# Optimization experiments

Hardware: AMD Instinct MI355X
Metric: run time of the kernel (lower is better)

The kernel has to match this reference:

```python
import jax, jax.numpy as jnp
import numpy as np

GH, GW = 8, 8  # hypernetwork patch grid
EPS = 1e-5


def image_coords(b, h, w, dtype):
    # matches get_image_coordinates: channel0 = x (varies along W), channel1 = y (varies along H)
    xs = jnp.linspace(-1.0, 1.0, w, dtype=dtype)
    ys = jnp.linspace(-1.0, 1.0, h, dtype=dtype)
    X = jnp.broadcast_to(xs[None, :], (h, w))
    Y = jnp.broadcast_to(ys[:, None], (h, w))
    g = jnp.stack([X, Y], axis=0)  # [2,H,W]
    return jnp.broadcast_to(g[None], (b, 2, h, w))


def im2col3(x):
    # reflect-pad 3x3 im2col -> [B,C,9,H,W]
    H, W = x.shape[2], x.shape[3]
    xp = jnp.pad(x, ((0, 0), (0, 0), (1, 1), (1, 1)), mode='reflect')
    cols = [xp[:, :, i:i + H, j:j + W] for i in range(3) for j in range(3)]
    return jnp.stack(cols, axis=2)


def meta_dw3(x, wsig):
    # depthwise 3x3 conv with per-patch weights. wsig: [B, C*9, GH, GW]
    B, C, H, W = x.shape
    p, q = H // GH, W // GW
    cols = im2col3(x).reshape(B, C, 9, GH, p, GW, q)
    Wd = wsig.reshape(B, C, 9, GH, GW)
    out = jnp.einsum('bctuivj,bctuv->bcuivj', cols, Wd)
    return out.reshape(B, C, H, W)


def meta_pw(x, wsig, out_nc):
    # pointwise 1x1 conv with per-patch weights. wsig: [B, out_nc*C, GH, GW]
    B, C, H, W = x.shape
    p, q = H // GH, W // GW
    xr = x.reshape(B, C, GH, p, GW, q)
    Wp = wsig.reshape(B, out_nc, C, GH, GW)
    out = jnp.einsum('bcuivj,bocuv->bouivj', xr, Wp)
    return out.reshape(B, out_nc, H, W)


def batch_norm(x, g, b):
    m = jnp.mean(x, (0, 2, 3), keepdims=True)
    v = jnp.var(x, (0, 2, 3), keepdims=True)
    return (x - m) * jax.lax.rsqrt(v + EPS) * g[None, :, None, None] + b[None, :, None, None]


def relu6(x):
    return jnp.clip(x, 0.0, 6.0)


def hpir(x, wsig, out_nc, g_dw, b_dw, g_pw, b_pw):
    # HyperPatchInvertedResidual, expand_ratio=1, stride=1, in_nc != out_nc -> no residual
    C = x.shape[1]
    n_dw = C * 9
    h = relu6(batch_norm(meta_dw3(x, wsig[:, :n_dw]), g_dw, b_dw))
    h = batch_norm(meta_pw(h, wsig[:, n_dw:n_dw + out_nc * C], out_nc), g_pw, b_pw)
    return h


def resize_bilinear(p, hw):
    B, C = p.shape[0], p.shape[1]
    return jax.image.resize(p, (B, C, hw[0], hw[1]), method='bilinear')


def decoder_forward(x_img, f0, f1, w0, w1, w2,
                    g_dw0, b_dw0, g_pw0, b_pw0,
                    g_dw1, b_dw1, g_pw1, b_pw1,
                    g_dw2, b_dw2, g_pw2, b_pw2):
    feats = [x_img, f0, f1]  # [img] + features[:-1]
    level_w = [w0, w1, w2]
    level_out = [64, 32, 21]
    bn_p = [(g_dw0, b_dw0, g_pw0, b_pw0),
            (g_dw1, b_dw1, g_pw1, b_pw1),
            (g_dw2, b_dw2, g_pw2, b_pw2)]
    p = None
    for level in range(3):
        f = feats[-level - 1]
        if p is None:
            p = f
        else:
            if p.shape[2:] != f.shape[2:]:
                p = resize_bilinear(p, f.shape[2:])
            p = jnp.concatenate([f, p], axis=1)
        B, _, H, W = p.shape
        p = jnp.concatenate([image_coords(B, H, W, p.dtype), p], axis=1)
        g_dw, b_dw, g_pw, b_pw = bn_p[level]
        p = hpir(p, level_w[level], level_out[level], g_dw, b_dw, g_pw, b_pw)
    return p


def setup_inputs() -> dict:
    key = jax.random.key(0)
    ks = jax.random.split(key, 8)
    inp = {
        'x_img': jax.random.normal(ks[0], (4, 3, 256, 256), jnp.float32),
        'f0': jax.random.normal(ks[1], (4, 32, 64, 64), jnp.float32),
        'f1': jax.random.normal(ks[2], (4, 64, 32, 32), jnp.float32),
        'w0': jax.random.normal(ks[3], (4, 4818, 8, 8), jnp.float32) * 0.1,
        'w1': jax.random.normal(ks[4], (4, 4018, 8, 8), jnp.float32) * 0.1,
        'w2': jax.random.normal(ks[5], (4, 1110, 8, 8), jnp.float32) * 0.1,
    }
    for name, c in [('dw0', 66), ('pw0', 64), ('dw1', 98), ('pw1', 32), ('dw2', 37), ('pw2', 21)]:
        inp['g_' + name] = jnp.ones((c,), jnp.float32)
        inp['b_' + name] = jnp.zeros((c,), jnp.float32)
    return inp


def reference(x_img, f0, f1, w0, w1, w2,
              g_dw0, b_dw0, g_pw0, b_pw0,
              g_dw1, b_dw1, g_pw1, b_pw1,
              g_dw2, b_dw2, g_pw2, b_pw2):
    return decoder_forward(x_img, f0, f1, w0, w1, w2,
                           g_dw0, b_dw0, g_pw0, b_pw0,
                           g_dw1, b_dw1, g_pw1, b_pw1,
                           g_dw2, b_dw2, g_pw2, b_pw2)
```

## Files before the change

kernel.cpp:

```cpp
#include <hip/hip_runtime.h>

#define EPS 1e-5f

__device__ __forceinline__ int reflect_idx(int i, int n) {
    if (i < 0) return -i;
    if (i >= n) return 2 * n - 2 - i;
    return i;
}

__device__ __forceinline__ float bilin(const float* __restrict__ pb, int Hp, float sy, float sx) {
    int y0 = (int)floorf(sy), x0 = (int)floorf(sx);
    float fy = sy - y0, fx = sx - x0;
    int y0c = min(max(y0, 0), Hp - 1), y1c = min(max(y0 + 1, 0), Hp - 1);
    int x0c = min(max(x0, 0), Hp - 1), x1c = min(max(x0 + 1, 0), Hp - 1);
    float v00 = pb[y0c * Hp + x0c], v01 = pb[y0c * Hp + x1c];
    float v10 = pb[y1c * Hp + x0c], v11 = pb[y1c * Hp + x1c];
    return v00 * (1 - fy) * (1 - fx) + v01 * (1 - fy) * fx
         + v10 * fy * (1 - fx) + v11 * fy * fx;
}

template <int C>
__device__ __forceinline__ void reduce_ss_wide(const float* __restrict__ part,
                                               const float* __restrict__ g,
                                               const float* __restrict__ bb,
                                               float* ss, float* scratch,
                                               float invN, int tid) {
    constexpr int G = 256 / C;
    int grp = tid / C;
    int c = tid - grp * C;
    if (grp < G) {
        float s1 = 0.f, s2 = 0.f;
        for (int s = grp; s < 64; s += G) {
            s1 += part[s * 2 * C + 2 * c];
            s2 += part[s * 2 * C + 2 * c + 1];
        }
        scratch[grp * 2 * C + 2 * c] = s1;
        scratch[grp * 2 * C + 2 * c + 1] = s2;
    }
    __syncthreads();
    if (tid < C) {
        float s1 = 0.f, s2 = 0.f;
#pragma unroll
        for (int gg = 0; gg < G; ++gg) {
            s1 += scratch[gg * 2 * C + 2 * tid];
            s2 += scratch[gg * 2 * C + 2 * tid + 1];
        }
        float m = s1 * invN;
        float var = s2 * invN - m * m;
        float sc = g[tid] * rsqrtf(var + EPS);
        ss[2 * tid] = sc;
        ss[2 * tid + 1] = bb[tid] - m * sc;
    }
    __syncthreads();
}

__global__ __launch_bounds__(256)
void wtrans_kernel(const float* __restrict__ w2, float* __restrict__ wT) {
    int uv = blockIdx.x & 63, b = blockIdx.x >> 6;
    const float* src = w2 + (size_t)b * 1110 * 64 + uv;
    float* dst = wT + ((size_t)(b * 64 + uv)) * 1110;
    for (int i = threadIdx.x; i < 1110; i += 256) dst[i] = src[(size_t)i * 64];
}

template <int LEVEL, bool WRITE>
__global__ __launch_bounds__(256)
void fused_dw_kernel(const float* __restrict__ feat, const float* __restrict__ prev,
                     const float* __restrict__ part_prev, const float* __restrict__ g_prev,
                     const float* __restrict__ b_prev, float invN_prev,
                     const float* __restrict__ wsig,
                     float* __restrict__ out, float* __restrict__ part) {
    constexpr int C    = LEVEL == 0 ? 66 : 98;
    constexpr int H    = LEVEL == 0 ? 32 : 64;
    constexpr int TILE = 16;
    constexpr int NT   = H / TILE;
    constexpr int PXPT = (TILE * TILE) / 256;
    constexpr int WC   = LEVEL == 0 ? 4818 : 4018;
    constexpr int NF   = LEVEL == 0 ? 64 : 32;
    constexpr int Hp   = LEVEL == 1 ? 32 : 64;
    constexpr int Cp   = LEVEL == 1 ? 64 : 32;
    constexpr int P    = H / 8;
    constexpr float SC = 0.5f;
    constexpr int HS   = TILE + 2;
    constexpr int PSS  = (LEVEL == 0) ? 2 : 2 * Cp;

    __shared__ float sh[HS * HS];
    __shared__ float pssl[PSS];
    __shared__ float scratch[512];
    int tid = threadIdx.x, bid = blockIdx.x;
    int tile = bid % (NT * NT);
    int c = (bid / (NT * NT)) % C;
    int b = bid / (NT * NT * C);
    int ty0 = (tile / NT) * TILE, tx0 = (tile % NT) * TILE;

    if constexpr (LEVEL != 0) {
        reduce_ss_wide<Cp>(part_prev, g_prev, b_prev, pssl, scratch, invN_prev, tid);
    }

    for (int i = tid; i < HS * HS; i += 256) {
        int h = reflect_idx(ty0 - 1 + i / HS, H);
        int w = reflect_idx(tx0 - 1 + i % HS, H);
        float val;
        if (c == 0)      val = -1.f + 2.f * w / (H - 1);
        else if (c == 1) val = -1.f + 2.f * h / (H - 1);
        else if (c < 2 + NF) val = feat[((size_t)(b * NF + c - 2) * H + h) * H + w];
        else {
            int o = c - 2 - NF;
            const float* pb = prev + (size_t)(b * Cp + o) * Hp * Hp;
            float raw = bilin(pb, Hp, (h + 0.5f) * SC - 0.5f, (w + 0.5f) * SC - 0.5f);
            val = raw * pssl[2 * o] + pssl[2 * o + 1];
        }
        sh[i] = val;
    }
    __syncthreads();

    float s1 = 0.f, s2 = 0.f;
    float* ob = out + (((size_t)(b * C + c)) * H + ty0) * H + tx0;
    float wreg[9];
    if constexpr (TILE == P) {
        const float* wb = wsig + ((size_t)(b * WC + c * 9)) * 64 + (ty0 / P) * 8 + (tx0 / P);
#pragma unroll
        for (int t = 0; t < 9; ++t) wreg[t] = wb[(size_t)t * 64];
    }
#pragma unroll
    for (int k = 0; k < PXPT; ++k) {
        int px = tid + k * 256;
        int tyy = px / TILE, txx = px % TILE;
        if constexpr (TILE != P) {
            int u = (ty0 + tyy) / P, vv = (tx0 + txx) / P;
            const float* wb = wsig + ((size_t)(b * WC + c * 9)) * 64 + u * 8 + vv;
#pragma unroll
            for (int t = 0; t < 9; ++t) wreg[t] = wb[(size_t)t * 64];
        }
        float acc = 0.f;
#pragma unroll
        for (int t = 0; t < 9; ++t)
            acc += wreg[t] * sh[(tyy + t / 3) * HS + txx + t % 3];
        if constexpr (WRITE) ob[tyy * H + txx] = acc;
        s1 += acc; s2 += acc * acc;
    }
#pragma unroll
    for (int off = 32; off; off >>= 1) {
        s1 += __shfl_xor(s1, off);
        s2 += __shfl_xor(s2, off);
    }
    __shared__ float r1[4], r2[4];
    int wave = tid >> 6;
    if ((tid & 63) == 0) { r1[wave] = s1; r2[wave] = s2; }
    __syncthreads();
    if (tid == 0) {
        int slot = bid & 63;
        atomicAdd(&part[slot * 2 * C + 2 * c],     r1[0] + r1[1] + r1[2] + r1[3]);
        atomicAdd(&part[slot * 2 * C + 2 * c + 1], r2[0] + r2[1] + r2[2] + r2[3]);
    }
}

__global__ __launch_bounds__(256)
void dw2_col_kernel(const float* __restrict__ ximg, const float* __restrict__ prev,
                    const float* __restrict__ part_prev, const float* __restrict__ g_prev,
                    const float* __restrict__ b_prev,
                    const float* __restrict__ wT,
                    float* __restrict__ out, float* __restrict__ part) {
    const int C = 37, H = 256, W = 256, Hp = 64, Cp = 32;
    const int S = 260;
    __shared__ float sh[10 * S];
    __shared__ float pssl[64];
    __shared__ float lwv[72];
    __shared__ float scratch[512];
    __shared__ float r1[4], r2[4];

    int tid = threadIdx.x, bid = blockIdx.x;
    int rb = bid & 31;
    int c  = (bid >> 5) % C;
    int b  = bid / (32 * C);
    int ty0 = rb * 8;
    int u = rb >> 2;

    if (tid < 72) {
        int v = tid / 9, t = tid - v * 9;
        lwv[tid] = wT[((size_t)(b * 64 + u * 8 + v)) * 1110 + c * 9 + t];
    }
    reduce_ss_wide<32>(part_prev, g_prev, b_prev, pssl, scratch, 1.f / 16384.f, tid);

    const float* pb = (c >= 5) ? prev + (size_t)(b * Cp + (c - 5)) * Hp * Hp : nullptr;
    const float* xrow = (c >= 2 && c < 5) ? ximg + (size_t)(b * 3 + c - 2) * H * W : nullptr;
    float cx = -1.f + tid * (2.f / 255.f);
    float sxm = (tid + 0.5f) * 0.25f - 0.5f;
    int x0m = (int)floorf(sxm);
    float fxm = sxm - x0m;
    int x0cm = min(max(x0m, 0), Hp - 1), x1cm = min(max(x0m + 1, 0), Hp - 1);

#pragma unroll
    for (int r = 0; r < 10; ++r) {
        int h = reflect_idx(ty0 - 1 + r, H);
        float val;
        if (c == 0)      val = cx;
        else if (c == 1) val = -1.f + h * (2.f / 255.f);
        else if (c < 5)  val = xrow[h * W + tid];
        else {
            float sy = (h + 0.5f) * 0.25f - 0.5f;
            int y0 = (int)floorf(sy);
            float fy = sy - y0;
            int y0c = min(max(y0, 0), Hp - 1), y1c = min(max(y0 + 1, 0), Hp - 1);
            const float* q0 = pb + y0c * Hp;
            const float* q1 = pb + y1c * Hp;
            float a0 = q0[x0cm] + (q0[x1cm] - q0[x0cm]) * fxm;
            float a1 = q1[x0cm] + (q1[x1cm] - q1[x0cm]) * fxm;
            float raw = a0 + (a1 - a0) * fy;
            val = raw * pssl[2 * (c - 5)] + pssl[2 * (c - 5) + 1];
        }
        sh[r * S + tid + 1] = val;
    }
    if (tid < 20) {
        int r = tid >> 1, side = tid & 1;
        int wimg = side ? 254 : 1;
        int h = reflect_idx(ty0 - 1 + r, H);
        float val;
        if (c == 0)      val = -1.f + wimg * (2.f / 255.f);
        else if (c == 1) val = -1.f + h * (2.f / 255.f);
        else if (c < 5)  val = xrow[h * W + wimg];
        else {
            float sx = (wimg + 0.5f) * 0.25f - 0.5f;
            int x0 = (int)floorf(sx); float fx = sx - x0;
            int x0c = min(max(x0, 0), Hp - 1), x1c = min(max(x0 + 1, 0), Hp - 1);
            float sy = (h + 0.5f) * 0.25f - 0.5f;
            int y0 = (int)floorf(sy); float fy = sy - y0;
            int y0c = min(max(y0, 0), Hp - 1), y1c = min(max(y0 + 1, 0), Hp - 1);
            const float* q0 = pb + y0c * Hp;
            const float* q1 = pb + y1c * Hp;
            float a0 = q0[x0c] + (q0[x1c] - q0[x0c]) * fx;
            float a1 = q1[x0c] + (q1[x1c] - q1[x0c]) * fx;
            float raw = a0 + (a1 - a0) * fy;
            val = raw * pssl[2 * (c - 5)] + pssl[2 * (c - 5) + 1];
        }
        sh[r * S + (side ? 257 : 0)] = val;
    }
    __syncthreads();

    int t = tid;
    int v = t >> 5;
    float wr[9];
#pragma unroll
    for (int tap = 0; tap < 9; ++tap) wr[tap] = lwv[v * 9 + tap];

    float px[8];
#pragma unroll
    for (int k = 0; k < 8; ++k) px[k] = 0.f;

#pragma unroll
    for (int r = 0; r < 10; ++r) {
        float L = sh[r * S + t];
        float M = sh[r * S + t + 1];
        float R = sh[r * S + t + 2];
#pragma unroll
        for (int dr = 0; dr < 3; ++dr) {
            int k = r - dr;
            if (k >= 0 && k < 8)
                px[k] += wr[dr * 3] * L + wr[dr * 3 + 1] * M + wr[dr * 3 + 2] * R;
        }
    }

    float* ob = out + (((size_t)(b * C + c)) * H + ty0) * W + t;
    float s1 = 0.f, s2 = 0.f;
#pragma unroll
    for (int k = 0; k < 8; ++k) {
        ob[k * W] = px[k];
        s1 += px[k]; s2 += px[k] * px[k];
    }
#pragma unroll
    for (int off = 32; off; off >>= 1) {
        s1 += __shfl_xor(s1, off);
        s2 += __shfl_xor(s2, off);
    }
    int wave = tid >> 6;
    if ((tid & 63) == 0) { r1[wave] = s1; r2[wave] = s2; }
    __syncthreads();
    if (tid == 0) {
        int slot = bid & 63;
        atomicAdd(&part[slot * 2 * C + 2 * c],     r1[0] + r1[1] + r1[2] + r1[3]);
        atomicAdd(&part[slot * 2 * C + 2 * c + 1], r2[0] + r2[1] + r2[2] + r2[3]);
    }
}

template <int C, int ONC, int H, int PX_T, int OC_T>
__global__ __launch_bounds__(256)
void pw_small_kernel(const float* __restrict__ x, const float* __restrict__ wsig,
                     const float* __restrict__ part_in, const float* __restrict__ g,
                     const float* __restrict__ bb, float invN,
                     float* __restrict__ out, float* __restrict__ part, int WC, int ndw) {
    constexpr int P = H / 8;
    constexpr int OC_I = ONC / OC_T;
    __shared__ float lw[ONC * C];
    __shared__ float lx[C * PX_T];
    __shared__ float ssl[2 * C];
    __shared__ float scratch[512];
    int tid = threadIdx.x, bid = blockIdx.x;
    int uv = bid & 63, b = bid >> 6;
    int u = uv >> 3, v = uv & 7;

    const size_t wbase = ((size_t)b * WC + ndw) * 64 + uv;
    for (int i = tid; i < ONC * C; i += 256) lw[i] = wsig[wbase + (size_t)i * 64];
    reduce_ss_wide<C>(part_in, g, bb, ssl, scratch, invN, tid);

    for (int i = tid; i < C * PX_T; i += 256) {
        int c = i / PX_T, pxl = i % PX_T;
        int h = u * P + pxl / P, w = v * P + pxl % P;
        float xv = x[(((size_t)b * C + c) * H + h) * H + w];
        lx[i] = fminf(fmaxf(xv * ssl[2 * c] + ssl[2 * c + 1], 0.f), 6.f);
    }
    __syncthreads();

    int px_id = tid % PX_T, oc_id = tid / PX_T;
    int h = u * P + px_id / P, w = v * P + px_id % P;
    float acc[OC_I];
#pragma unroll
    for (int oi = 0; oi < OC_I; ++oi) acc[oi] = 0.f;
    for (int c = 0; c < C; ++c) {
        float xv = lx[c * PX_T + px_id];
#pragma unroll
        for (int oi = 0; oi < OC_I; ++oi)
            acc[oi] += lw[(oc_id * OC_I + oi) * C + c] * xv;
    }
    float* ob = out + (((size_t)b * ONC) * H + h) * H + w;
#pragma unroll
    for (int oi = 0; oi < OC_I; ++oi)
        ob[(size_t)(oc_id * OC_I + oi) * H * H] = acc[oi];

    constexpr int GROUP = (PX_T < 64) ? PX_T : 64;
    int lane = tid & 63;
    int slot = bid & 63;
#pragma unroll
    for (int oi = 0; oi < OC_I; ++oi) {
        float s1 = acc[oi], s2 = acc[oi] * acc[oi];
#pragma unroll
        for (int off = GROUP / 2; off; off >>= 1) {
            s1 += __shfl_xor(s1, off);
            s2 += __shfl_xor(s2, off);
        }
        if ((lane & (GROUP - 1)) == 0) {
            int o = oc_id * OC_I + oi;
            atomicAdd(&part[slot * 2 * ONC + 2 * o], s1);
            atomicAdd(&part[slot * 2 * ONC + 2 * o + 1], s2);
        }
    }
}

__global__ __launch_bounds__(256)
void pw2_kernel(const float* __restrict__ x, const float* __restrict__ wT,
                const float* __restrict__ part_in, const float* __restrict__ g,
                const float* __restrict__ bb,
                float* __restrict__ out, float* __restrict__ part) {
    const int C = 37, ONC = 21, H = 256;
    __shared__ float lw[777];
    __shared__ float ssl[74];
    __shared__ float scratch[512];
    __shared__ float r1[4][ONC], r2[4][ONC];
    int tid = threadIdx.x, bid = blockIdx.x;
    int chunk = bid & 3;
    int uv = (bid >> 2) & 63;
    int b = bid >> 8;
    int y0 = (uv >> 3) * 32 + chunk * 8, x0 = (uv & 7) * 32;

    const float* wt = wT + ((size_t)(b * 64 + uv)) * 1110 + 333;
    for (int i = tid; i < 777; i += 256) lw[i] = wt[i];
    reduce_ss_wide<37>(part_in, g, bb, ssl, scratch, 1.f / 262144.f, tid);

    int row = tid >> 5, col = tid & 31;
    const float* xb = x + (((size_t)(b * C)) * H + y0 + row) * H + x0 + col;
    float acc[ONC];
#pragma unroll
    for (int o = 0; o < ONC; ++o) acc[o] = 0.f;

    for (int c = 0; c < C; ++c) {
        float xv = xb[(size_t)c * H * H];
        xv = fminf(fmaxf(xv * ssl[2 * c] + ssl[2 * c + 1], 0.f), 6.f);
#pragma unroll
        for (int o = 0; o < ONC; ++o)
            acc[o] += lw[o * C + c] * xv;
    }
    float* ob = out + (((size_t)(b * ONC)) * H + y0 + row) * H + x0 + col;
#pragma unroll
    for (int o = 0; o < ONC; ++o) ob[(size_t)o * H * H] = acc[o];

    int wave = tid >> 6, lane = tid & 63;
#pragma unroll
    for (int o = 0; o < ONC; ++o) {
        float s1 = acc[o], s2 = acc[o] * acc[o];
#pragma unroll
        for (int off = 32; off; off >>= 1) {
            s1 += __shfl_xor(s1, off);
            s2 += __shfl_xor(s2, off);
        }
        if (lane == 0) { r1[wave][o] = s1; r2[wave][o] = s2; }
    }
    __syncthreads();
    int slot = bid & 63;
    for (int o = tid; o < ONC; o += 256) {
        atomicAdd(&part[slot * 42 + 2 * o],     r1[0][o] + r1[1][o] + r1[2][o] + r1[3][o]);
        atomicAdd(&part[slot * 42 + 2 * o + 1], r2[0][o] + r2[1][o] + r2[2][o] + r2[3][o]);
    }
}

__global__ __launch_bounds__(256)
void finalbn_kernel(float* __restrict__ out, const float* __restrict__ part_in,
                    const float* __restrict__ g, const float* __restrict__ bb) {
    __shared__ float ssl[42];
    __shared__ float scratch[512];
    reduce_ss_wide<21>(part_in, g, bb, ssl, scratch, 1.f / 262144.f, threadIdx.x);
    const int total4 = 4 * 21 * 256 * 256 / 4;
    for (int idx = blockIdx.x * 256 + threadIdx.x; idx < total4; idx += gridDim.x * 256) {
        int c = (idx / (256 * 256 / 4)) % 21;
        float4 v = ((float4*)out)[idx];
        float sc = ssl[2 * c], sb = ssl[2 * c + 1];
        v.x = v.x * sc + sb; v.y = v.y * sc + sb; v.z = v.z * sc + sb; v.w = v.w * sc + sb;
        ((float4*)out)[idx] = v;
    }
}

extern "C" void kernel_launch(void* const* d_in, const int* in_sizes, int n_in,
                              void* d_out, int out_size, void* d_ws, size_t ws_size,
                              hipStream_t stream) {
    const float* x_img = (const float*)d_in[0];
    const float* f0    = (const float*)d_in[1];
    const float* f1    = (const float*)d_in[2];
    const float* w0    = (const float*)d_in[3];
    const float* w1    = (const float*)d_in[4];
    const float* w2    = (const float*)d_in[5];
    const float* g_dw0 = (const float*)d_in[6],  *b_dw0 = (const float*)d_in[7];
    const float* g_pw0 = (const float*)d_in[8],  *b_pw0 = (const float*)d_in[9];
    const float* g_dw1 = (const float*)d_in[10], *b_dw1 = (const float*)d_in[11];
    const float* g_pw1 = (const float*)d_in[12], *b_pw1 = (const float*)d_in[13];
    const float* g_dw2 = (const float*)d_in[14], *b_dw2 = (const float*)d_in[15];
    const float* g_pw2 = (const float*)d_in[16], *b_pw2 = (const float*)d_in[17];
    float* out = (float*)d_out;
    float* ws = (float*)d_ws;

    float* part_dw0 = ws;
    float* part_pw0 = ws + 8448;
    float* part_dw1 = ws + 16640;
    float* part_pw1 = ws + 29184;
    float* part_dw2 = ws + 33280;
    float* part_pw2 = ws + 38016;
    float* wT     = ws + 40704;
    float* pw0raw = ws + 324864;
    float* pw1raw = pw0raw + 262144;
    float* bigA   = pw1raw + 524288;

    hipMemsetAsync(ws, 0, 40704 * sizeof(float), stream);
    wtrans_kernel<<<256, 256, 0, stream>>>(w2, wT);

    fused_dw_kernel<0, true><<<4 * 66 * 4, 256, 0, stream>>>(
        f1, nullptr, nullptr, nullptr, nullptr, 0.f, w0, bigA, part_dw0);
    pw_small_kernel<66, 64, 32, 16, 16><<<256, 256, 0, stream>>>(
        bigA, w0, part_dw0, g_dw0, b_dw0, 1.f / 4096.f, pw0raw, part_pw0, 4818, 594);
    fused_dw_kernel<1, true><<<4 * 98 * 16, 256, 0, stream>>>(
        f0, pw0raw, part_pw0, g_pw0, b_pw0, 1.f / 4096.f, w1, bigA, part_dw1);
    pw_small_kernel<98, 32, 64, 64, 4><<<256, 256, 0, stream>>>(
        bigA, w1, part_dw1, g_dw1, b_dw1, 1.f / 16384.f, pw1raw, part_pw1, 4018, 882);
    dw2_col_kernel<<<4 * 37 * 32, 256, 0, stream>>>(
        x_img, pw1raw, part_pw1, g_pw1, b_pw1, wT, bigA, part_dw2);
    pw2_kernel<<<1024, 256, 0, stream>>>(bigA, wT, part_dw2, g_dw2, b_dw2, out, part_pw2);
    finalbn_kernel<<<1024, 256, 0, stream>>>(out, part_pw2, g_pw2, b_pw2);
}
```

Before: 157.8 us.

## Merge weight transpose into dw0, register-only dw2, bf16 intermediate for pw2

Folds the w2 transpose kernel into the level-0 depthwise launch as extra blocks, removing one launch. Rewrites the level-2 depthwise kernel so each thread computes its left, middle and right columns directly in registers. This drops the shared-memory halo tile, the block-wide BN reduction and the __syncthreads; the BN scale and shift now come from a wave-level shuffle, and partial sums are issued per wave. The 37-channel 256x256 intermediate is stored as bf16 to halve its write and read traffic in pw2, which reduces precision of that activation. The register version recomputes bilinear samples about three times per pixel.

After: 157.7 us. No clear change (-0.0%).

```diff
diff --git a/kernel.cpp b/kernel.cpp
--- a/kernel.cpp
+++ b/kernel.cpp
@@ -1,4 +1,5 @@
 #include <hip/hip_runtime.h>
+#include <hip/hip_bf16.h>
 
 #define EPS 1e-5f
 
@@ -54,21 +55,14 @@
     __syncthreads();
 }
 
-__global__ __launch_bounds__(256)
-void wtrans_kernel(const float* __restrict__ w2, float* __restrict__ wT) {
-    int uv = blockIdx.x & 63, b = blockIdx.x >> 6;
-    const float* src = w2 + (size_t)b * 1110 * 64 + uv;
-    float* dst = wT + ((size_t)(b * 64 + uv)) * 1110;
-    for (int i = threadIdx.x; i < 1110; i += 256) dst[i] = src[(size_t)i * 64];
-}
-
-template <int LEVEL, bool WRITE>
-__global__ __launch_bounds__(256)
-void fused_dw_kernel(const float* __restrict__ feat, const float* __restrict__ prev,
-                     const float* __restrict__ part_prev, const float* __restrict__ g_prev,
-                     const float* __restrict__ b_prev, float invN_prev,
-                     const float* __restrict__ wsig,
-                     float* __restrict__ out, float* __restrict__ part) {
+template <int LEVEL>
+__device__ __forceinline__
+void fused_dw_body(int bid, int tid,
+                   const float* __restrict__ feat, const float* __restrict__ prev,
+                   const float* __restrict__ part_prev, const float* __restrict__ g_prev,
+                   const float* __restrict__ b_prev, float invN_prev,
+                   const float* __restrict__ wsig,
+                   float* __restrict__ out, float* __restrict__ part) {
     constexpr int C    = LEVEL == 0 ? 66 : 98;
     constexpr int H    = LEVEL == 0 ? 32 : 64;
     constexpr int TILE = 16;
@@ -76,8 +70,8 @@
     constexpr int PXPT = (TILE * TILE) / 256;
     constexpr int WC   = LEVEL == 0 ? 4818 : 4018;
     constexpr int NF   = LEVEL == 0 ? 64 : 32;
-    constexpr int Hp   = LEVEL == 1 ? 32 : 64;
-    constexpr int Cp   = LEVEL == 1 ? 64 : 32;
+    constexpr int Hp   = 32;
+    constexpr int Cp   = 64;
     constexpr int P    = H / 8;
     constexpr float SC = 0.5f;
     constexpr int HS   = TILE + 2;
@@ -86,7 +80,6 @@
     __shared__ float sh[HS * HS];
     __shared__ float pssl[PSS];
     __shared__ float scratch[512];
-    int tid = threadIdx.x, bid = blockIdx.x;
     int tile = bid % (NT * NT);
     int c = (bid / (NT * NT)) % C;
     int b = bid / (NT * NT * C);
@@ -135,7 +128,7 @@
 #pragma unroll
         for (int t = 0; t < 9; ++t)
             acc += wreg[t] * sh[(tyy + t / 3) * HS + txx + t % 3];
-        if constexpr (WRITE) ob[tyy * H + txx] = acc;
+        ob[tyy * H + txx] = acc;
         s1 += acc; s2 += acc * acc;
     }
 #pragma unroll
@@ -155,115 +148,131 @@
 }
 
 __global__ __launch_bounds__(256)
-void dw2_col_kernel(const float* __restrict__ ximg, const float* __restrict__ prev,
+void dw0_prep_kernel(const float* __restrict__ f1, const float* __restrict__ w0,
+                     float* __restrict__ out, float* __restrict__ part,
+                     const float* __restrict__ w2, float* __restrict__ wT) {
+    int bid = blockIdx.x;
+    if (bid < 256) {
+        int uv = bid & 63, b = bid >> 6;
+        const float* src = w2 + (size_t)b * 1110 * 64 + uv;
+        float* dst = wT + ((size_t)(b * 64 + uv)) * 1110;
+        for (int i = threadIdx.x; i < 1110; i += 256) dst[i] = src[(size_t)i * 64];
+        return;
+    }
+    fused_dw_body<0>(bid - 256, threadIdx.x, f1, nullptr, nullptr, nullptr, nullptr, 0.f,
+                     w0, out, part);
+}
+
+__global__ __launch_bounds__(256)
+void fused_dw1_kernel(const float* __restrict__ feat, const float* __restrict__ prev,
+                      const float* __restrict__ part_prev, const float* __restrict__ g_prev,
+                      const float* __restrict__ b_prev, float invN_prev,
+                      const float* __restrict__ wsig,
+                      float* __restrict__ out, float* __restrict__ part) {
+    fused_dw_body<1>(blockIdx.x, threadIdx.x, feat, prev, part_prev, g_prev, b_prev,
+                     invN_prev, wsig, out, part);
+}
+
+__global__ __launch_bounds__(256)
+void dw2_reg_kernel(const float* __restrict__ ximg, const float* __restrict__ prev,
                     const float* __restrict__ part_prev, const float* __restrict__ g_prev,
                     const float* __restrict__ b_prev,
                     const float* __restrict__ wT,
-                    float* __restrict__ out, float* __restrict__ part) {
+                    __hip_bfloat16* __restrict__ outb, float* __restrict__ part) {
     const int C = 37, H = 256, W = 256, Hp = 64, Cp = 32;
-    const int S = 260;
-    __shared__ float sh[10 * S];
-    __shared__ float pssl[64];
-    __shared__ float lwv[72];
-    __shared__ float scratch[512];
-    __shared__ float r1[4], r2[4];
-
     int tid = threadIdx.x, bid = blockIdx.x;
     int rb = bid & 31;
     int c  = (bid >> 5) % C;
     int b  = bid / (32 * C);
     int ty0 = rb * 8;
     int u = rb >> 2;
-
-    if (tid < 72) {
-        int v = tid / 9, t = tid - v * 9;
-        lwv[tid] = wT[((size_t)(b * 64 + u * 8 + v)) * 1110 + c * 9 + t];
-    }
-    reduce_ss_wide<32>(part_prev, g_prev, b_prev, pssl, scratch, 1.f / 16384.f, tid);
-
-    const float* pb = (c >= 5) ? prev + (size_t)(b * Cp + (c - 5)) * Hp * Hp : nullptr;
-    const float* xrow = (c >= 2 && c < 5) ? ximg + (size_t)(b * 3 + c - 2) * H * W : nullptr;
-    float cx = -1.f + tid * (2.f / 255.f);
-    float sxm = (tid + 0.5f) * 0.25f - 0.5f;
-    int x0m = (int)floorf(sxm);
-    float fxm = sxm - x0m;
-    int x0cm = min(max(x0m, 0), Hp - 1), x1cm = min(max(x0m + 1, 0), Hp - 1);
+    int t = tid;
+    int lane = tid & 63;
+
+    float psc = 0.f, psh = 0.f;
+    if (c >= 5) {
+        int o = c - 5;
+        float s1 = part_prev[lane * 2 * Cp + 2 * o];
+        float s2 = part_prev[lane * 2 * Cp + 2 * o + 1];
+#pragma unroll
+        for (int off = 32; off; off >>= 1) {
+            s1 += __shfl_xor(s1, off);
+            s2 += __shfl_xor(s2, off);
+        }
+        float m = s1 * (1.f / 16384.f);
+        float var = s2 * (1.f / 16384.f) - m * m;
+        psc = g_prev[o] * rsqrtf(var + EPS);
+        psh = b_prev[o] - m * psc;
+    }
+
+    int v = t >> 5;
+    float wr[9];
+    const float* wt = wT + ((size_t)(b * 64 + u * 8 + v)) * 1110 + c * 9;
+#pragma unroll
+    for (int tap = 0; tap < 9; ++tap) wr[tap] = wt[tap];
+
+    int colL = (t == 0) ? 1 : t - 1;
+    int colM = t;
+    int colR = (t == 255) ? 254 : t + 1;
+
+    const float* pb   = (c >= 5) ? prev + (size_t)(b * Cp + (c - 5)) * Hp * Hp : nullptr;
+    const float* xim  = (c >= 2 && c < 5) ? ximg + (size_t)(b * 3 + c - 2) * H * W : nullptr;
+
+    float fxs[3]; int x0s[3], x1s[3]; float cxs[3];
+    int cols[3] = {colL, colM, colR};
+#pragma unroll
+    for (int j = 0; j < 3; ++j) {
+        float sx = (cols[j] + 0.5f) * 0.25f - 0.5f;
+        int x0 = (int)floorf(sx);
+        fxs[j] = sx - x0;
+        x0s[j] = min(max(x0, 0), Hp - 1);
+        x1s[j] = min(max(x0 + 1, 0), Hp - 1);
+        cxs[j] = -1.f + cols[j] * (2.f / 255.f);
+    }
+
+    float px[8];
+#pragma unroll
+    for (int k = 0; k < 8; ++k) px[k] = 0.f;
 
 #pragma unroll
     for (int r = 0; r < 10; ++r) {
         int h = reflect_idx(ty0 - 1 + r, H);
-        float val;
-        if (c == 0)      val = cx;
-        else if (c == 1) val = -1.f + h * (2.f / 255.f);
-        else if (c < 5)  val = xrow[h * W + tid];
-        else {
+        float bv[3];
+        if (c == 0) {
+            bv[0] = cxs[0]; bv[1] = cxs[1]; bv[2] = cxs[2];
+        } else if (c == 1) {
+            float cy = -1.f + h * (2.f / 255.f);
+            bv[0] = cy; bv[1] = cy; bv[2] = cy;
+        } else if (c < 5) {
+            const float* row = xim + h * W;
+            bv[0] = row[colL]; bv[1] = row[colM]; bv[2] = row[colR];
+        } else {
             float sy = (h + 0.5f) * 0.25f - 0.5f;
             int y0 = (int)floorf(sy);
             float fy = sy - y0;
             int y0c = min(max(y0, 0), Hp - 1), y1c = min(max(y0 + 1, 0), Hp - 1);
             const float* q0 = pb + y0c * Hp;
             const float* q1 = pb + y1c * Hp;
-            float a0 = q0[x0cm] + (q0[x1cm] - q0[x0cm]) * fxm;
-            float a1 = q1[x0cm] + (q1[x1cm] - q1[x0cm]) * fxm;
-            float raw = a0 + (a1 - a0) * fy;
-            val = raw * pssl[2 * (c - 5)] + pssl[2 * (c - 5) + 1];
-        }
-        sh[r * S + tid + 1] = val;
-    }
-    if (tid < 20) {
-        int r = tid >> 1, side = tid & 1;
-        int wimg = side ? 254 : 1;
-        int h = reflect_idx(ty0 - 1 + r, H);
-        float val;
-        if (c == 0)      val = -1.f + wimg * (2.f / 255.f);
-        else if (c == 1) val = -1.f + h * (2.f / 255.f);
-        else if (c < 5)  val = xrow[h * W + wimg];
-        else {
-            float sx = (wimg + 0.5f) * 0.25f - 0.5f;
-            int x0 = (int)floorf(sx); float fx = sx - x0;
-            int x0c = min(max(x0, 0), Hp - 1), x1c = min(max(x0 + 1, 0), Hp - 1);
-            float sy = (h + 0.5f) * 0.25f - 0.5f;
-            int y0 = (int)floorf(sy); float fy = sy - y0;
-            int y0c = min(max(y0, 0), Hp - 1), y1c = min(max(y0 + 1, 0), Hp - 1);
-            const float* q0 = pb + y0c * Hp;
-            const float* q1 = pb + y1c * Hp;
-            float a0 = q0[x0c] + (q0[x1c] - q0[x0c]) * fx;
-            float a1 = q1[x0c] + (q1[x1c] - q1[x0c]) * fx;
-            float raw = a0 + (a1 - a0) * fy;
-            val = raw * pssl[2 * (c - 5)] + pssl[2 * (c - 5) + 1];
-        }
-        sh[r * S + (side ? 257 : 0)] = val;
-    }
-    __syncthreads();
-
-    int t = tid;
-    int v = t >> 5;
-    float wr[9];
-#pragma unroll
-    for (int tap = 0; tap < 9; ++tap) wr[tap] = lwv[v * 9 + tap];
-
-    float px[8];
-#pragma unroll
-    for (int k = 0; k < 8; ++k) px[k] = 0.f;
-
-#pragma unroll
-    for (int r = 0; r < 10; ++r) {
-        float L = sh[r * S + t];
-        float M = sh[r * S + t + 1];
-        float R = sh[r * S + t + 2];
+#pragma unroll
+            for (int j = 0; j < 3; ++j) {
+                float a0 = q0[x0s[j]] + (q0[x1s[j]] - q0[x0s[j]]) * fxs[j];
+                float a1 = q1[x0s[j]] + (q1[x1s[j]] - q1[x0s[j]]) * fxs[j];
+                bv[j] = (a0 + (a1 - a0) * fy) * psc + psh;
+            }
+        }
 #pragma unroll
         for (int dr = 0; dr < 3; ++dr) {
             int k = r - dr;
             if (k >= 0 && k < 8)
-                px[k] += wr[dr * 3] * L + wr[dr * 3 + 1] * M + wr[dr * 3 + 2] * R;
-        }
-    }
-
-    float* ob = out + (((size_t)(b * C + c)) * H + ty0) * W + t;
+                px[k] += wr[dr * 3] * bv[0] + wr[dr * 3 + 1] * bv[1] + wr[dr * 3 + 2] * bv[2];
+        }
+    }
+
+    __hip_bfloat16* ob = outb + (((size_t)(b * C + c)) * H + ty0) * W + t;
     float s1 = 0.f, s2 = 0.f;
 #pragma unroll
     for (int k = 0; k < 8; ++k) {
-        ob[k * W] = px[k];
+        ob[k * W] = __float2bfloat16(px[k]);
         s1 += px[k]; s2 += px[k] * px[k];
     }
 #pragma unroll
@@ -271,13 +280,10 @@
         s1 += __shfl_xor(s1, off);
         s2 += __shfl_xor(s2, off);
     }
-    int wave = tid >> 6;
-    if ((tid & 63) == 0) { r1[wave] = s1; r2[wave] = s2; }
-    __syncthreads();
-    if (tid == 0) {
+    if (lane == 0) {
         int slot = bid & 63;
-        atomicAdd(&part[slot * 2 * C + 2 * c],     r1[0] + r1[1] + r1[2] + r1[3]);
-        atomicAdd(&part[slot * 2 * C + 2 * c + 1], r2[0] + r2[1] + r2[2] + r2[3]);
+        atomicAdd(&part[slot * 2 * C + 2 * c],     s1);
+        atomicAdd(&part[slot * 2 * C + 2 * c + 1], s2);
     }
 }
 
@@ -345,7 +351,7 @@
 }
 
 __global__ __launch_bounds__(256)
-void pw2_kernel(const float* __restrict__ x, const float* __restrict__ wT,
+void pw2_kernel(const __hip_bfloat16* __restrict__ x, const float* __restrict__ wT,
                 const float* __restrict__ part_in, const float* __restrict__ g,
                 const float* __restrict__ bb,
                 float* __restrict__ out, float* __restrict__ part) {
@@ -365,13 +371,13 @@
     reduce_ss_wide<37>(part_in, g, bb, ssl, scratch, 1.f / 262144.f, tid);
 
     int row = tid >> 5, col = tid & 31;
-    const float* xb = x + (((size_t)(b * C)) * H + y0 + row) * H + x0 + col;
+    const __hip_bfloat16* xb = x + (((size_t)(b * C)) * H + y0 + row) * H + x0 + col;
     float acc[ONC];
 #pragma unroll
     for (int o = 0; o < ONC; ++o) acc[o] = 0.f;
 
     for (int c = 0; c < C; ++c) {
-        float xv = xb[(size_t)c * H * H];
+        float xv = __bfloat162float(xb[(size_t)c * H * H]);
         xv = fminf(fmaxf(xv * ssl[2 * c] + ssl[2 * c + 1], 0.f), 6.f);
 #pragma unroll
         for (int o = 0; o < ONC; ++o)
@@ -444,20 +450,19 @@
     float* pw0raw = ws + 324864;
     float* pw1raw = pw0raw + 262144;
     float* bigA   = pw1raw + 524288;
+    __hip_bfloat16* bigAb = (__hip_bfloat16*)bigA;
 
     hipMemsetAsync(ws, 0, 40704 * sizeof(float), stream);
-    wtrans_kernel<<<256, 256, 0, stream>>>(w2, wT);
-
-    fused_dw_kernel<0, true><<<4 * 66 * 4, 256, 0, stream>>>(
-        f1, nullptr, nullptr, nullptr, nullptr, 0.f, w0, bigA, part_dw0);
+
+    dw0_prep_kernel<<<256 + 4 * 66 * 4, 256, 0, stream>>>(f1, w0, bigA, part_dw0, w2, wT);
     pw_small_kernel<66, 64, 32, 16, 16><<<256, 256, 0, stream>>>(
         bigA, w0, part_dw0, g_dw0, b_dw0, 1.f / 4096.f, pw0raw, part_pw0, 4818, 594);
-    fused_dw_kernel<1, true><<<4 * 98 * 16, 256, 0, stream>>>(
+    fused_dw1_kernel<<<4 * 98 * 16, 256, 0, stream>>>(
         f0, pw0raw, part_pw0, g_pw0, b_pw0, 1.f / 4096.f, w1, bigA, part_dw1);
     pw_small_kernel<98, 32, 64, 64, 4><<<256, 256, 0, stream>>>(
         bigA, w1, part_dw1, g_dw1, b_dw1, 1.f / 16384.f, pw1raw, part_pw1, 4018, 882);
-    dw2_col_kernel<<<4 * 37 * 32, 256, 0, stream>>>(
-        x_img, pw1raw, part_pw1, g_pw1, b_pw1, wT, bigA, part_dw2);
-    pw2_kernel<<<1024, 256, 0, stream>>>(bigA, wT, part_dw2, g_dw2, b_dw2, out, part_pw2);
+    dw2_reg_kernel<<<4 * 37 * 32, 256, 0, stream>>>(
+        x_img, pw1raw, part_pw1, g_pw1, b_pw1, wT, bigAb, part_dw2);
+    pw2_kernel<<<1024, 256, 0, stream>>>(bigAb, wT, part_dw2, g_dw2, b_dw2, out, part_pw2);
     finalbn_kernel<<<1024, 256, 0, stream>>>(out, part_pw2, g_pw2, b_pw2);
 }
```
